# Kernel tuning notes

Measured on AMD Instinct MI355X. Metric: run time of the kernel, lower is better.

Reference implementation:

```python
import jax, jax.numpy as jnp
import numpy as np

N = 50000      # nodes of type 'student'
E = 625000     # edges per relation
H = 128        # hidden_channels
C = 6          # num_classes
F_IN = 3       # hardcoded num_features in the module


def setup_inputs() -> dict:
    key = jax.random.key(0)
    ks = jax.random.split(key, 32)
    s = 0.05
    d = {}
    d["x_student"] = jax.random.normal(ks[0], (N, F_IN), dtype=jnp.float32)
    d["ei_friend"] = jax.random.randint(ks[1], (2, E), 0, N)
    d["ei_study"] = jax.random.randint(ks[2], (2, E), 0, N)
    # embedding Linear(3 -> H)
    d["emb_w"] = jax.random.normal(ks[3], (F_IN, H), dtype=jnp.float32) * s
    d["emb_b"] = jnp.zeros((H,), jnp.float32)
    # per-layer, per-edge-type RGCNConv params: relation-0 weight, root weight, bias
    i = 4
    for l in range(2):
        for e in ("f", "s"):
            d[f"w_rel_{l}_{e}"] = jax.random.normal(ks[i], (H, H), dtype=jnp.float32) * s; i += 1
            d[f"w_root_{l}_{e}"] = jax.random.normal(ks[i], (H, H), dtype=jnp.float32) * s; i += 1
            d[f"b_{l}_{e}"] = jnp.zeros((H,), jnp.float32)
    # output Linear(H -> C)
    d["out_w"] = jax.random.normal(ks[i], (H, C), dtype=jnp.float32) * s
    d["out_b"] = jnp.zeros((C,), jnp.float32)
    return d


def _rgcn_conv(h, ei, w_rel, w_root, b):
    # PyG RGCNConv with edge_type==0 everywhere: mean-aggregate src features at dst,
    # project by relation-0 weight, add root transform and bias.
    src, dst = ei[0], ei[1]
    msg = h[src]                                             # [E, H] gather
    agg = jax.ops.segment_sum(msg, dst, num_segments=N)      # [N, H]
    deg = jax.ops.segment_sum(jnp.ones((ei.shape[1],), h.dtype), dst, num_segments=N)
    agg = agg / jnp.maximum(deg, 1.0)[:, None]               # mean aggr (0 for isolated nodes)
    return agg @ w_rel + h @ w_root + b


def reference(x_student, ei_friend, ei_study, emb_w, emb_b,
              w_rel_0_f, w_root_0_f, b_0_f, w_rel_0_s, w_root_0_s, b_0_s,
              w_rel_1_f, w_root_1_f, b_1_f, w_rel_1_s, w_root_1_s, b_1_s,
              out_w, out_b):
    h = jax.nn.relu(x_student @ emb_w + emb_b)
    # layer 0: sum over the two relations, divide by valid_edge_count=2, relu (dropout eval=no-op)
    acc = _rgcn_conv(h, ei_friend, w_rel_0_f, w_root_0_f, b_0_f) \
        + _rgcn_conv(h, ei_study, w_rel_0_s, w_root_0_s, b_0_s)
    h = jax.nn.relu(acc / 2.0)
    # layer 1 (last): no relu/dropout
    acc = _rgcn_conv(h, ei_friend, w_rel_1_f, w_root_1_f, b_1_f) \
        + _rgcn_conv(h, ei_study, w_rel_1_s, w_root_1_s, b_1_s)
    h = acc / 2.0
    return h @ out_w + out_b
```

## Files before the change

### kernel.cpp

```cpp
#include <hip/hip_runtime.h>

#define NN 50000
#define NE 625000
#define HD 128
#define CAP 40
#define ZROW NN
#define WFL (12*8*64*8)
#define WFH (6*8*64*8)
#define DPC 6250
#define BINCAP 80000

typedef __attribute__((ext_vector_type(8))) short short8;
typedef __attribute__((ext_vector_type(4))) float f32x4;
typedef __attribute__((ext_vector_type(4))) unsigned uint4v;

__device__ __forceinline__ unsigned short f2bf(float f) {
    unsigned u = __builtin_bit_cast(unsigned, f);
    u += 0x7FFFu + ((u >> 16) & 1u);
    return (unsigned short)(u >> 16);
}
__device__ __forceinline__ unsigned pack2(float lo, float hi) {
    return (unsigned)f2bf(lo) | ((unsigned)f2bf(hi) << 16);
}
__device__ __forceinline__ float bflo(unsigned v) { unsigned u = v << 16; return __builtin_bit_cast(float, u); }
__device__ __forceinline__ float bfhi(unsigned v) { unsigned u = v & 0xFFFF0000u; return __builtin_bit_cast(float, u); }

__device__ __forceinline__ void extract8(uint4v u, int j0, int cnt, unsigned* out) {
    unsigned raw[8];
    raw[0] = u.x & 0xFFFFu; raw[1] = u.x >> 16;
    raw[2] = u.y & 0xFFFFu; raw[3] = u.y >> 16;
    raw[4] = u.z & 0xFFFFu; raw[5] = u.z >> 16;
    raw[6] = u.w & 0xFFFFu; raw[7] = u.w >> 16;
    #pragma unroll
    for (int j = 0; j < 8; ++j) out[j] = (j0 + j < cnt) ? raw[j] : ZROW;
}

__global__ __launch_bounds__(256) void k_p1(
    const float* __restrict__ x, const float* __restrict__ w,
    const float* __restrict__ b, unsigned* __restrict__ h0, unsigned* __restrict__ h1,
    const int* __restrict__ ei_f, const int* __restrict__ ei_s,
    int* __restrict__ cursor, unsigned* __restrict__ bin,
    const float* __restrict__ wrf0, const float* __restrict__ wtf0, const float* __restrict__ bf0,
    const float* __restrict__ wrs0, const float* __restrict__ wts0, const float* __restrict__ bs0,
    const float* __restrict__ wrf1, const float* __restrict__ wtf1, const float* __restrict__ bf1,
    const float* __restrict__ wrs1, const float* __restrict__ wts1, const float* __restrict__ bs1,
    unsigned short* __restrict__ Wf, float* __restrict__ bcat)
{
    __shared__ int hist[8], base[8], ofs[8];
    int bid = blockIdx.x, t = threadIdx.x;
    if (bid < 490) {
        int rel = bid >= 245;
        int chunk = bid - rel * 245;
        const int* ei = rel ? ei_s : ei_f;
        if (t < 8) { hist[t] = 0; ofs[t] = 0; }
        __syncthreads();
        int cls[10], dloc[10], srcv[10];
        int e0 = chunk * 2560 + t;
        #pragma unroll
        for (int i = 0; i < 10; ++i) {
            int e = e0 + i * 256;
            if (e < NE) {
                int d = ei[NE + e];
                int s = ei[e];
                int c = d / DPC;
                cls[i] = c; dloc[i] = d - c * DPC; srcv[i] = s;
                atomicAdd(&hist[c], 1);
            } else cls[i] = -1;
        }
        __syncthreads();
        if (t < 8) base[t] = atomicAdd(&cursor[rel * 8 + t], hist[t]);
        __syncthreads();
        #pragma unroll
        for (int i = 0; i < 10; ++i) {
            if (cls[i] >= 0) {
                int p = atomicAdd(&ofs[cls[i]], 1);
                unsigned idx = (unsigned)(base[cls[i]] + p);
                if (idx < BINCAP)
                    bin[(long)(rel * 8 + cls[i]) * BINCAP + idx] =
                        ((unsigned)dloc[i] << 16) | (unsigned)srcv[i];
            }
        }
    } else if (bid < 12990) {
        int i = (bid - 490) * 256 + t;
        int n = i >> 6, c = (i & 63) * 2;
        float x0 = x[n*3+0], x1 = x[n*3+1], x2 = x[n*3+2];
        float v0 = fmaf(x0, w[c],   fmaf(x1, w[HD+c],   fmaf(x2, w[2*HD+c],   b[c])));
        float v1 = fmaf(x0, w[c+1], fmaf(x1, w[HD+c+1], fmaf(x2, w[2*HD+c+1], b[c+1])));
        v0 = fmaxf(v0, 0.f); v1 = fmaxf(v1, 0.f);
        h0[i] = pack2(v0, v1);
    } else if (bid == 12990) {
        if (t < 64)       h0[(long)ZROW*64 + t] = 0u;
        else if (t < 128) h1[(long)ZROW*64 + (t - 64)] = 0u;
    } else {
        int i = (bid - 12991) * 256 + t;
        int ln = i / 384, k = i - ln * 384;
        int l = ln >> 7, n = ln & 127;
        const float* wrf = l ? wrf1 : wrf0;
        const float* wrs = l ? wrs1 : wrs0;
        const float* wtf = l ? wtf1 : wtf0;
        const float* wts = l ? wts1 : wts0;
        float v;
        if (k < 128)      v = wrf[k*HD + n];
        else if (k < 256) v = wrs[(k-128)*HD + n];
        else              v = wtf[(k-256)*HD + n] + wts[(k-256)*HD + n];
        int nt = n >> 4, m16 = n & 15;
        int kc = k >> 5, rem = k & 31, quad = rem >> 3, j = rem & 7;
        int lane = quad * 16 + m16;
        Wf[(long)(((l*12 + kc)*8 + nt)*64 + lane)*8 + j] = f2bf(0.5f * v);
        if (i < 256) {
            int ll = i >> 7, cc = i & 127;
            const float* bfp = ll ? bf1 : bf0;
            const float* bsp = ll ? bs1 : bs0;
            bcat[i] = 0.5f * (bfp[cc] + bsp[cc]);
        }
    }
}

__global__ __launch_bounds__(256) void k_p2(
    const int* __restrict__ cursor, const unsigned* __restrict__ bin,
    int* __restrict__ degF, int* __restrict__ degS,
    unsigned short* __restrict__ bktF, unsigned short* __restrict__ bktS)
{
    int bid = blockIdx.x, t = threadIdx.x;
    int rel = bid >= 504;
    int bq = bid - rel * 504;
    int cls = bq & 7;
    int chunk = bq >> 3;
    int cnt = min(cursor[rel * 8 + cls], BINCAP);
    const unsigned* bp = bin + (long)(rel * 8 + cls) * BINCAP;
    int* deg = rel ? degS : degF;
    unsigned short* bkt = rel ? bktS : bktF;
    const int dbase = cls * DPC;
    int e0 = chunk * 1280 + t;
    #pragma unroll
    for (int i = 0; i < 5; ++i) {
        int e = e0 + i * 256;
        if (e < cnt) {
            unsigned en = bp[e];
            int src = en & 0xFFFFu;
            int dst = dbase + (int)(en >> 16);
            int pos = atomicAdd(&deg[dst], 1);
            if (pos < CAP) bkt[(long)dst * CAP + pos] = (unsigned short)src;
        }
    }
}

__global__ __launch_bounds__(256) void k_spmm(
    const unsigned* __restrict__ h,
    const int* __restrict__ degF, const int* __restrict__ degS,
    const unsigned short* __restrict__ bktF, const unsigned short* __restrict__ bktS,
    unsigned* __restrict__ aggF, unsigned* __restrict__ aggS)
{
    int w = threadIdx.x >> 6, lane = threadIdx.x & 63;
    int n = blockIdx.x * 4 + w;
    int dF = degF[n], dS = degS[n];
    int cF = min(dF, CAP), cS = min(dS, CAP);
    const unsigned short* rowF = bktF + (long)n*CAP;
    const unsigned short* rowS = bktS + (long)n*CAP;
    uint4v uF0 = *(const uint4v*)(rowF);
    uint4v uF1 = *(const uint4v*)(rowF + 8);
    uint4v uS0 = *(const uint4v*)(rowS);
    uint4v uS1 = *(const uint4v*)(rowS + 8);
    unsigned iF[16], iS[16];
    extract8(uF0, 0, cF, iF); extract8(uF1, 8, cF, iF + 8);
    extract8(uS0, 0, cS, iS); extract8(uS1, 8, cS, iS + 8);
    unsigned vF[16], vS[16];
    #pragma unroll
    for (int j = 0; j < 16; ++j) vF[j] = h[iF[j]*64u + lane];
    #pragma unroll
    for (int j = 0; j < 16; ++j) vS[j] = h[iS[j]*64u + lane];
    float aF0 = 0.f, aF1 = 0.f, aS0 = 0.f, aS1 = 0.f;
    #pragma unroll
    for (int j = 0; j < 16; ++j) { aF0 += bflo(vF[j]); aF1 += bfhi(vF[j]); }
    #pragma unroll
    for (int j = 0; j < 16; ++j) { aS0 += bflo(vS[j]); aS1 += bfhi(vS[j]); }
    for (int j = 16; j < cF; j += 8) {
        uint4v u = *(const uint4v*)(rowF + j);
        unsigned ii[8];
        extract8(u, j, cF, ii);
        unsigned vv[8];
        #pragma unroll
        for (int q = 0; q < 8; ++q) vv[q] = h[ii[q]*64u + lane];
        #pragma unroll
        for (int q = 0; q < 8; ++q) { aF0 += bflo(vv[q]); aF1 += bfhi(vv[q]); }
    }
    for (int j = 16; j < cS; j += 8) {
        uint4v u = *(const uint4v*)(rowS + j);
        unsigned ii[8];
        extract8(u, j, cS, ii);
        unsigned vv[8];
        #pragma unroll
        for (int q = 0; q < 8; ++q) vv[q] = h[ii[q]*64u + lane];
        #pragma unroll
        for (int q = 0; q < 8; ++q) { aS0 += bflo(vv[q]); aS1 += bfhi(vv[q]); }
    }
    float invF = 1.f / fmaxf((float)dF, 1.f);
    float invS = 1.f / fmaxf((float)dS, 1.f);
    aggF[n*64 + lane] = pack2(aF0*invF, aF1*invF);
    aggS[n*64 + lane] = pack2(aS0*invS, aS1*invS);
}

__global__ __launch_bounds__(256) void k_gemm(
    const unsigned short* __restrict__ A0, const unsigned short* __restrict__ A1,
    const unsigned short* __restrict__ A2,
    const unsigned short* __restrict__ Wf, const float* __restrict__ bias,
    unsigned short* __restrict__ outH, int mode,
    const float* __restrict__ ow, const float* __restrict__ ob,
    float* __restrict__ out6)
{
    __shared__ unsigned short Bs[WFH];
    const int t = threadIdx.x;
    const int wv = t >> 6, lane = t & 63;
    const int m16 = lane & 15, quad = lane >> 4;
    const int row0 = blockIdx.x * 64 + wv * 16;
    const int r = row0 + m16;
    const bool valid = r < NN;
    f32x4 acc[8];
    #pragma unroll
    for (int nt = 0; nt < 8; ++nt) acc[nt] = (f32x4){0.f,0.f,0.f,0.f};

    #pragma unroll
    for (int ph = 0; ph < 2; ++ph) {
        if (ph) __syncthreads();
        const uint4v* srcW = (const uint4v*)(Wf + (long)ph * WFH);
        uint4v* dstW = (uint4v*)Bs;
        #pragma unroll
        for (int i = 0; i < 12; ++i)
            dstW[i*256 + t] = srcW[i*256 + t];
        __syncthreads();
        #pragma unroll
        for (int kl = 0; kl < 6; ++kl) {
            int kc = ph*6 + kl;
            const unsigned short* src; int kofs;
            if (kc < 4)      { src = A0; kofs = kc*32; }
            else if (kc < 8) { src = A1; kofs = kc*32 - 128; }
            else             { src = A2; kofs = kc*32 - 256; }
            short8 a;
            if (valid) a = *(const short8*)(src + (long)r*HD + kofs + quad*8);
            else       a = short8{0,0,0,0,0,0,0,0};
            #pragma unroll
            for (int nt = 0; nt < 8; ++nt) {
                short8 bfr = *(const short8*)(Bs + ((kl*8 + nt)*64 + lane)*8);
                acc[nt] = __builtin_amdgcn_mfma_f32_16x16x32_bf16(a, bfr, acc[nt], 0, 0, 0);
            }
        }
    }

    float bs[8];
    #pragma unroll
    for (int nt = 0; nt < 8; ++nt) bs[nt] = bias[nt*16 + m16];

    if (mode == 0) {
        #pragma unroll
        for (int reg = 0; reg < 4; ++reg) {
            int rr = row0 + quad*4 + reg;
            if (rr >= NN) continue;
            #pragma unroll
            for (int nt = 0; nt < 8; ++nt) {
                float v = fmaxf(acc[nt][reg] + bs[nt], 0.f);
                outH[(long)rr*HD + nt*16 + m16] = f2bf(v);
            }
        }
    } else {
        float owr[8][6];
        #pragma unroll
        for (int nt = 0; nt < 8; ++nt) {
            int c = nt*16 + m16;
            #pragma unroll
            for (int j = 0; j < 6; ++j) owr[nt][j] = ow[c*6 + j];
        }
        #pragma unroll
        for (int reg = 0; reg < 4; ++reg) {
            int rr = row0 + quad*4 + reg;
            float tj[6] = {0,0,0,0,0,0};
            #pragma unroll
            for (int nt = 0; nt < 8; ++nt) {
                float hv = acc[nt][reg] + bs[nt];
                #pragma unroll
                for (int j = 0; j < 6; ++j) tj[j] = fmaf(hv, owr[nt][j], tj[j]);
            }
            #pragma unroll
            for (int mask = 1; mask < 16; mask <<= 1)
                #pragma unroll
                for (int j = 0; j < 6; ++j) tj[j] += __shfl_xor(tj[j], mask, 64);
            if (m16 == 0 && rr < NN) {
                #pragma unroll
                for (int j = 0; j < 6; ++j) out6[(long)rr*6 + j] = tj[j] + ob[j];
            }
        }
    }
}

extern "C" void kernel_launch(void* const* d_in, const int* in_sizes, int n_in,
                              void* d_out, int out_size, void* d_ws, size_t ws_size,
                              hipStream_t stream)
{
    const float* x     = (const float*)d_in[0];
    const int*   ei_f  = (const int*)d_in[1];
    const int*   ei_s  = (const int*)d_in[2];
    const float* emb_w = (const float*)d_in[3];
    const float* emb_b = (const float*)d_in[4];
    const float* wr0f  = (const float*)d_in[5];
    const float* wt0f  = (const float*)d_in[6];
    const float* b0f   = (const float*)d_in[7];
    const float* wr0s  = (const float*)d_in[8];
    const float* wt0s  = (const float*)d_in[9];
    const float* b0s   = (const float*)d_in[10];
    const float* wr1f  = (const float*)d_in[11];
    const float* wt1f  = (const float*)d_in[12];
    const float* b1f   = (const float*)d_in[13];
    const float* wr1s  = (const float*)d_in[14];
    const float* wt1s  = (const float*)d_in[15];
    const float* b1s   = (const float*)d_in[16];
    const float* out_w = (const float*)d_in[17];
    const float* out_b = (const float*)d_in[18];
    float* out = (float*)d_out;

    char* ws = (char*)d_ws;
    size_t off = 0;
    auto alloc = [&](size_t bytes) { char* p = ws + off; off += (bytes + 255) & ~255ULL; return p; };
    unsigned* h0   = (unsigned*)alloc((size_t)(NN+1)*64*4);
    unsigned* h1   = (unsigned*)alloc((size_t)(NN+1)*64*4);
    unsigned* aggF = (unsigned*)alloc((size_t)NN*64*4);
    unsigned* aggS = (unsigned*)alloc((size_t)NN*64*4);
    int*   degF = (int*)alloc((size_t)NN*4);
    int*   degS = (int*)alloc((size_t)NN*4);
    int*   cursor = (int*)alloc((size_t)16*4);
    unsigned short* bktF = (unsigned short*)alloc((size_t)NN*CAP*2);
    unsigned short* bktS = (unsigned short*)alloc((size_t)NN*CAP*2);
    unsigned short* Wf = (unsigned short*)alloc((size_t)2*WFL*2);
    float* bcat = (float*)alloc((size_t)2*HD*4);
    unsigned* bin = (unsigned*)alloc((size_t)16*BINCAP*4);

    size_t degpad = ((size_t)NN*4 + 255) & ~255ULL;
    hipMemsetAsync(degF, 0, degpad*2 + 64, stream);

    k_p1<<<13375, 256, 0, stream>>>(x, emb_w, emb_b, h0, h1,
                                    ei_f, ei_s, cursor, bin,
                                    wr0f, wt0f, b0f, wr0s, wt0s, b0s,
                                    wr1f, wt1f, b1f, wr1s, wt1s, b1s,
                                    Wf, bcat);
    k_p2<<<1008, 256, 0, stream>>>(cursor, bin, degF, degS, bktF, bktS);
    k_spmm<<<NN/4, 256, 0, stream>>>(h0, degF, degS, bktF, bktS, aggF, aggS);
    k_gemm<<<(NN + 63)/64, 256, 0, stream>>>((const unsigned short*)aggF, (const unsigned short*)aggS,
                                             (const unsigned short*)h0, Wf, bcat,
                                             (unsigned short*)h1, 0, out_w, out_b, out);
    k_spmm<<<NN/4, 256, 0, stream>>>(h1, degF, degS, bktF, bktS, aggF, aggS);
    k_gemm<<<(NN + 63)/64, 256, 0, stream>>>((const unsigned short*)aggF, (const unsigned short*)aggS,
                                             (const unsigned short*)h1, Wf + WFL, bcat + HD,
                                             (unsigned short*)h1, 1, out_w, out_b, out);
}
```

Baseline: 276.4 us.

## Build CSR buckets in LDS per destination sub-range, write out coalesced

The second binning pass now gives each block a sub-range of 782 destinations within one class. The block scans the whole class bin, builds the degree counts and neighbor buckets in shared memory, then writes them to global memory in full coalesced stores. This replaces scattered global atomics and writes, and the memset of the degree arrays goes away. In exchange each block rereads its whole class bin (8x redundant reads) and only 128 blocks are launched. The first pass also reuses the histogram atomic's return value as the slot offset instead of running a second atomic pass.

```diff
diff --git a/kernel.cpp b/kernel.cpp
--- a/kernel.cpp
+++ b/kernel.cpp
@@ -8,6 +8,7 @@
 #define WFL (12*8*64*8)
 #define WFH (6*8*64*8)
 #define DPC 6250
+#define SUBD 782
 #define BINCAP 80000
 
 typedef __attribute__((ext_vector_type(8))) short short8;
@@ -46,15 +47,15 @@
     const float* __restrict__ wrs1, const float* __restrict__ wts1, const float* __restrict__ bs1,
     unsigned short* __restrict__ Wf, float* __restrict__ bcat)
 {
-    __shared__ int hist[8], base[8], ofs[8];
+    __shared__ int hist[8], base[8];
     int bid = blockIdx.x, t = threadIdx.x;
     if (bid < 490) {
         int rel = bid >= 245;
         int chunk = bid - rel * 245;
         const int* ei = rel ? ei_s : ei_f;
-        if (t < 8) { hist[t] = 0; ofs[t] = 0; }
+        if (t < 8) hist[t] = 0;
         __syncthreads();
-        int cls[10], dloc[10], srcv[10];
+        int cls[10], pp[10]; unsigned pk[10];
         int e0 = chunk * 2560 + t;
         #pragma unroll
         for (int i = 0; i < 10; ++i) {
@@ -63,8 +64,9 @@
                 int d = ei[NE + e];
                 int s = ei[e];
                 int c = d / DPC;
-                cls[i] = c; dloc[i] = d - c * DPC; srcv[i] = s;
-                atomicAdd(&hist[c], 1);
+                cls[i] = c;
+                pk[i] = ((unsigned)(d - c * DPC) << 16) | (unsigned)s;
+                pp[i] = atomicAdd(&hist[c], 1);
             } else cls[i] = -1;
         }
         __syncthreads();
@@ -73,11 +75,9 @@
         #pragma unroll
         for (int i = 0; i < 10; ++i) {
             if (cls[i] >= 0) {
-                int p = atomicAdd(&ofs[cls[i]], 1);
-                unsigned idx = (unsigned)(base[cls[i]] + p);
+                unsigned idx = (unsigned)(base[cls[i]] + pp[i]);
                 if (idx < BINCAP)
-                    bin[(long)(rel * 8 + cls[i]) * BINCAP + idx] =
-                        ((unsigned)dloc[i] << 16) | (unsigned)srcv[i];
+                    bin[(long)(rel * 8 + cls[i]) * BINCAP + idx] = pk[i];
             }
         }
     } else if (bid < 12990) {
@@ -121,28 +121,43 @@
     int* __restrict__ degF, int* __restrict__ degS,
     unsigned short* __restrict__ bktF, unsigned short* __restrict__ bktS)
 {
+    __shared__ unsigned short lbkt[SUBD * CAP];
+    __shared__ int ldeg[SUBD];
     int bid = blockIdx.x, t = threadIdx.x;
-    int rel = bid >= 504;
-    int bq = bid - rel * 504;
-    int cls = bq & 7;
-    int chunk = bq >> 3;
+    int cls = bid & 7;
+    int rel = (bid >> 3) & 1;
+    int sub = bid >> 4;
     int cnt = min(cursor[rel * 8 + cls], BINCAP);
     const unsigned* bp = bin + (long)(rel * 8 + cls) * BINCAP;
+    const int lo = sub * SUBD;
+    const int nd = min(SUBD, DPC - lo);
+    for (int j = t; j < nd; j += 256) ldeg[j] = 0;
+    __syncthreads();
+    for (int e0 = 0; e0 < cnt; e0 += 1024) {
+        unsigned en[4];
+        #pragma unroll
+        for (int q = 0; q < 4; ++q) {
+            int e = e0 + q * 256 + t;
+            en[q] = (e < cnt) ? bp[e] : 0xFFFFFFFFu;
+        }
+        #pragma unroll
+        for (int q = 0; q < 4; ++q) {
+            unsigned u = (en[q] >> 16) - (unsigned)lo;
+            if (u < (unsigned)nd) {
+                int p = atomicAdd(&ldeg[u], 1);
+                if (p < CAP) lbkt[u * CAP + p] = (unsigned short)(en[q] & 0xFFFFu);
+            }
+        }
+    }
+    __syncthreads();
+    const int gbase = cls * DPC + lo;
     int* deg = rel ? degS : degF;
     unsigned short* bkt = rel ? bktS : bktF;
-    const int dbase = cls * DPC;
-    int e0 = chunk * 1280 + t;
-    #pragma unroll
-    for (int i = 0; i < 5; ++i) {
-        int e = e0 + i * 256;
-        if (e < cnt) {
-            unsigned en = bp[e];
-            int src = en & 0xFFFFu;
-            int dst = dbase + (int)(en >> 16);
-            int pos = atomicAdd(&deg[dst], 1);
-            if (pos < CAP) bkt[(long)dst * CAP + pos] = (unsigned short)src;
-        }
-    }
+    for (int j = t; j < nd; j += 256) deg[gbase + j] = ldeg[j];
+    unsigned* gb = (unsigned*)(bkt + (long)gbase * CAP);
+    const unsigned* lb = (const unsigned*)lbkt;
+    const int ndw = nd * (CAP / 2);
+    for (int j = t; j < ndw; j += 256) gb[j] = lb[j];
 }
 
 __global__ __launch_bounds__(256) void k_spmm(
@@ -332,15 +347,14 @@
     float* bcat = (float*)alloc((size_t)2*HD*4);
     unsigned* bin = (unsigned*)alloc((size_t)16*BINCAP*4);
 
-    size_t degpad = ((size_t)NN*4 + 255) & ~255ULL;
-    hipMemsetAsync(degF, 0, degpad*2 + 64, stream);
+    hipMemsetAsync(cursor, 0, 16*4, stream);
 
     k_p1<<<13375, 256, 0, stream>>>(x, emb_w, emb_b, h0, h1,
                                     ei_f, ei_s, cursor, bin,
                                     wr0f, wt0f, b0f, wr0s, wt0s, b0s,
                                     wr1f, wt1f, b1f, wr1s, wt1s, b1s,
                                     Wf, bcat);
-    k_p2<<<1008, 256, 0, stream>>>(cursor, bin, degF, degS, bktF, bktS);
+    k_p2<<<128, 256, 0, stream>>>(cursor, bin, degF, degS, bktF, bktS);
     k_spmm<<<NN/4, 256, 0, stream>>>(h0, degF, degS, bktF, bktS, aggF, aggS);
     k_gemm<<<(NN + 63)/64, 256, 0, stream>>>((const unsigned short*)aggF, (const unsigned short*)aggS,
                                              (const unsigned short*)h0, Wf, bcat,
```

Measured after the change: 274.7 us. About the same (-0.6%).
